# Kernel tuning notes

Hardware: AMD Instinct MI355X
Metric: run time of the kernel (lower is better)

The kernel has to match this reference:

```python
import jax, jax.numpy as jnp
import numpy as np

HARDSHRINK_LAMBDA = 0.75

def setup_inputs() -> dict:
    key = jax.random.key(0)
    k1, k2, k3, k4, k5 = jax.random.split(key, 5)
    B, Cin, H, W = 32, 3, 128, 128
    Cmid, Dout = 256, 4096
    x = jax.random.normal(k1, (B, Cin, H, W), dtype=jnp.float32)
    # Conv2d(3,256,k=3,p=1) params, kaiming-ish scale
    conv_w = jax.random.normal(k2, (Cmid, Cin, 3, 3), dtype=jnp.float32) * (1.0 / np.sqrt(Cin * 9))
    conv_b = jax.random.normal(k3, (Cmid,), dtype=jnp.float32) * 0.01
    fc_w = jax.random.normal(k4, (Dout, Cmid), dtype=jnp.float32) * (1.0 / np.sqrt(Cmid))
    fc_b = jax.random.normal(k5, (Dout,), dtype=jnp.float32) * 0.01
    return {"x": x, "conv_w": conv_w, "conv_b": conv_b, "fc_w": fc_w, "fc_b": fc_b}

def reference(x, conv_w, conv_b, fc_w, fc_b):
    # Conv2d stride=1, padding=1  -> [B, Cmid, H, W]
    y = jax.lax.conv_general_dilated(
        x, conv_w, window_strides=(1, 1), padding=((1, 1), (1, 1)),
        dimension_numbers=("NCHW", "OIHW", "NCHW"))
    y = y + conv_b[None, :, None, None]
    y = jax.nn.relu(y)
    # Nearest upsample (integer scale) replicates each value s*s times; the
    # subsequent elementwise hardshrink then global average pool is therefore
    y = jnp.where(jnp.abs(y) > HARDSHRINK_LAMBDA, y, 0.0)
    pooled = jnp.mean(y, axis=(2, 3))  # [B, Cmid]
    out = pooled @ fc_w.T + fc_b       # [B, Dout]
    return jax.nn.log_sigmoid(out)
```

## Files before the change

kernel.cpp:

```cpp
#include <hip/hip_runtime.h>
#include <hip/hip_bf16.h>

#define LAMBDA 0.75f
#define CMID 256
#define DOUT 4096

typedef __attribute__((ext_vector_type(8))) short bf16x8;
typedef __attribute__((ext_vector_type(4))) float f32x4;

static inline __device__ short f2bf(float f) {
    __hip_bfloat16 h = __float2bfloat16(f);
    short s;
    __builtin_memcpy(&s, &h, 2);
    return s;
}

__global__ void zero_pooled(float* __restrict__ pooled) {
    int i = blockIdx.x * blockDim.x + threadIdx.x;
    if (i < 32 * CMID) pooled[i] = 0.f;
}

__global__ __launch_bounds__(256) void conv_pool_mfma(
    const float* __restrict__ x, const float* __restrict__ conv_w,
    const float* __restrict__ conv_b, float* __restrict__ pooled)
{
    __shared__ float xs[3 * 6 * 132];
    const int b  = blockIdx.x >> 5;
    const int h0 = (blockIdx.x & 31) * 4;
    const int t  = threadIdx.x;
    const int wv = t >> 6;
    const int l  = t & 63;
    const int lm = l & 15;
    const int g  = l >> 4;

    for (int i = t; i < 2376; i += 256) {
        int ci  = i / 792;
        int rem = i - ci * 792;
        int r   = rem / 132;
        int j   = rem - r * 132;
        int hh  = h0 - 1 + r;
        int col = j - 1;
        float v = 0.f;
        if ((unsigned)hh < 128u && (unsigned)col < 128u)
            v = x[(b * 3 + ci) * 16384 + hh * 128 + col];
        xs[i] = v;
    }

    bf16x8 afrag[4];
    f32x4  biasf[4];
    f32x4  pool[4];
    #pragma unroll
    for (int c = 0; c < 4; ++c) {
        const int ct = wv * 4 + c;
        const int co = ct * 16 + lm;
        const float* wp = conv_w + co * 27;
        float av[8];
        if (g < 3) {
            #pragma unroll
            for (int j = 0; j < 8; ++j) av[j] = wp[g * 9 + j];
        } else {
            av[0] = wp[8]; av[1] = wp[17]; av[2] = wp[26];
            av[3] = av[4] = av[5] = av[6] = av[7] = 0.f;
        }
        #pragma unroll
        for (int j = 0; j < 8; ++j) afrag[c][j] = f2bf(av[j]);
        #pragma unroll
        for (int r = 0; r < 4; ++r) {
            biasf[c][r] = conv_b[ct * 16 + 4 * g + r];
            pool[c][r]  = 0.f;
        }
    }

    int off[8];
    if (g < 3) {
        #pragma unroll
        for (int j = 0; j < 8; ++j)
            off[j] = g * 792 + (j / 3) * 132 + (j % 3) - 1;
    } else {
        off[0] = 0 * 792 + 2 * 132 + 1;
        off[1] = 1 * 792 + 2 * 132 + 1;
        off[2] = 2 * 792 + 2 * 132 + 1;
        off[3] = off[4] = off[5] = off[6] = off[7] = 0;
    }

    __syncthreads();

    #pragma unroll
    for (int rr = 0; rr < 4; ++rr) {
        const float* base = xs + rr * 132 + 1 + lm;
        #pragma unroll
        for (int tw = 0; tw < 8; ++tw) {
            float v[8];
            #pragma unroll
            for (int j = 0; j < 8; ++j) v[j] = base[off[j] + tw * 16];
            bf16x8 bfrag;
            #pragma unroll
            for (int j = 0; j < 8; ++j) bfrag[j] = f2bf(v[j]);
            #pragma unroll
            for (int c = 0; c < 4; ++c) {
                f32x4 acc = __builtin_amdgcn_mfma_f32_16x16x32_bf16(
                    afrag[c], bfrag, biasf[c], 0, 0, 0);
                #pragma unroll
                for (int r = 0; r < 4; ++r)
                    pool[c][r] += (acc[r] > LAMBDA) ? acc[r] : 0.f;
            }
        }
    }

    #pragma unroll
    for (int m = 1; m < 16; m <<= 1) {
        #pragma unroll
        for (int c = 0; c < 4; ++c)
            #pragma unroll
            for (int r = 0; r < 4; ++r)
                pool[c][r] += __shfl_xor(pool[c][r], m, 64);
    }
    if (lm == 0) {
        #pragma unroll
        for (int c = 0; c < 4; ++c)
            #pragma unroll
            for (int r = 0; r < 4; ++r)
                atomicAdd(&pooled[b * CMID + (wv * 4 + c) * 16 + 4 * g + r], pool[c][r]);
    }
}

__global__ __launch_bounds__(256) void fc_kernel(
    const float* __restrict__ pooled, const float* __restrict__ fc_w,
    const float* __restrict__ fc_b, float* __restrict__ out)
{
    __shared__ float pool[CMID];
    const int b = blockIdx.y;
    const int t = threadIdx.x;
    pool[t] = pooled[b * CMID + t] * (1.0f / 16384.0f);
    __syncthreads();

    const int d = blockIdx.x * 256 + t;
    const float4* wrow = (const float4*)(fc_w + d * CMID);
    float acc = fc_b[d];
    #pragma unroll 8
    for (int k4 = 0; k4 < CMID / 4; k4++) {
        float4 wv = wrow[k4];
        acc += wv.x * pool[k4 * 4 + 0] + wv.y * pool[k4 * 4 + 1]
             + wv.z * pool[k4 * 4 + 2] + wv.w * pool[k4 * 4 + 3];
    }
    float ls = fminf(acc, 0.f) - log1pf(expf(-fabsf(acc)));
    out[b * (int)DOUT + d] = ls;
}

extern "C" void kernel_launch(void* const* d_in, const int* in_sizes, int n_in,
                              void* d_out, int out_size, void* d_ws, size_t ws_size,
                              hipStream_t stream) {
    const float* x      = (const float*)d_in[0];
    const float* conv_w = (const float*)d_in[1];
    const float* conv_b = (const float*)d_in[2];
    const float* fc_w   = (const float*)d_in[3];
    const float* fc_b   = (const float*)d_in[4];
    float* out = (float*)d_out;

    float* pooled = (float*)d_ws;

    zero_pooled<<<32, 256, 0, stream>>>(pooled);
    conv_pool_mfma<<<32 * 32, 256, 0, stream>>>(x, conv_w, conv_b, pooled);
    fc_kernel<<<dim3(16, 32), 256, 0, stream>>>(pooled, fc_w, fc_b, out);
}
```

Before: 49.50 us.

## Build bf16 im2col tile in LDS and swap MFMA operand roles in conv-pool

The conv kernel now stages a packed bf16 im2col buffer in shared memory, one row per output pixel. Each MFMA B-fragment then comes from a single 16-byte LDS load instead of eight scalar loads and conversions per tile. Operands are swapped so pixels sit on the reduction side, which shrinks the lane reduction to two shuffles, and each block covers two rows instead of four to double the grid. The zero kernel is replaced by hipMemsetAsync, and launch bounds request four blocks per CU, at the cost of an extra LDS pass and sync.

```diff
diff --git a/kernel.cpp b/kernel.cpp
--- a/kernel.cpp
+++ b/kernel.cpp
@@ -10,45 +10,45 @@
 
 static inline __device__ short f2bf(float f) {
     __hip_bfloat16 h = __float2bfloat16(f);
-    short s;
-    __builtin_memcpy(&s, &h, 2);
+    short s; __builtin_memcpy(&s, &h, 2);
     return s;
 }
-
-__global__ void zero_pooled(float* __restrict__ pooled) {
-    int i = blockIdx.x * blockDim.x + threadIdx.x;
-    if (i < 32 * CMID) pooled[i] = 0.f;
+static inline __device__ unsigned pack2(float lo, float hi) {
+    unsigned a = (unsigned short)f2bf(lo);
+    unsigned b = (unsigned short)f2bf(hi);
+    return a | (b << 16);
 }
 
-__global__ __launch_bounds__(256) void conv_pool_mfma(
+__global__ __launch_bounds__(256, 4) void conv_pool_mfma(
     const float* __restrict__ x, const float* __restrict__ conv_w,
     const float* __restrict__ conv_b, float* __restrict__ pooled)
 {
-    __shared__ float xs[3 * 6 * 132];
-    const int b  = blockIdx.x >> 5;
-    const int h0 = (blockIdx.x & 31) * 4;
+    __shared__ float    raw[3 * 4 * 136];
+    __shared__ unsigned im2col[256 * 20];
+
+    const int b  = blockIdx.x >> 6;
+    const int h0 = (blockIdx.x & 63) * 2;
     const int t  = threadIdx.x;
+    const int l  = t & 63;
     const int wv = t >> 6;
-    const int l  = t & 63;
     const int lm = l & 15;
     const int g  = l >> 4;
 
-    for (int i = t; i < 2376; i += 256) {
-        int ci  = i / 792;
-        int rem = i - ci * 792;
-        int r   = rem / 132;
-        int j   = rem - r * 132;
+    for (int i = t; i < 1632; i += 256) {
+        int ci  = i / 544;
+        int rem = i - ci * 544;
+        int r   = rem / 136;
+        int idx = rem - r * 136;
         int hh  = h0 - 1 + r;
-        int col = j - 1;
+        int col = idx - 4;
         float v = 0.f;
         if ((unsigned)hh < 128u && (unsigned)col < 128u)
             v = x[(b * 3 + ci) * 16384 + hh * 128 + col];
-        xs[i] = v;
+        raw[i] = v;
     }
 
-    bf16x8 afrag[4];
-    f32x4  biasf[4];
-    f32x4  pool[4];
+    bf16x8 wfrag[4];
+    f32x4  biasf[4], pool[4];
     #pragma unroll
     for (int c = 0; c < 4; ++c) {
         const int ct = wv * 4 + c;
@@ -63,64 +63,61 @@
             av[3] = av[4] = av[5] = av[6] = av[7] = 0.f;
         }
         #pragma unroll
-        for (int j = 0; j < 8; ++j) afrag[c][j] = f2bf(av[j]);
-        #pragma unroll
-        for (int r = 0; r < 4; ++r) {
-            biasf[c][r] = conv_b[ct * 16 + 4 * g + r];
-            pool[c][r]  = 0.f;
-        }
+        for (int j = 0; j < 8; ++j) wfrag[c][j] = f2bf(av[j]);
+        const float bb = conv_b[co];
+        biasf[c] = (f32x4){bb, bb, bb, bb};
+        pool[c]  = (f32x4){0.f, 0.f, 0.f, 0.f};
     }
 
-    int off[8];
-    if (g < 3) {
+    __syncthreads();
+
+    {
+        const int out_r = t >> 7;
+        const int px    = t & 127;
+        unsigned q[16];
         #pragma unroll
-        for (int j = 0; j < 8; ++j)
-            off[j] = g * 792 + (j / 3) * 132 + (j % 3) - 1;
-    } else {
-        off[0] = 0 * 792 + 2 * 132 + 1;
-        off[1] = 1 * 792 + 2 * 132 + 1;
-        off[2] = 2 * 792 + 2 * 132 + 1;
-        off[3] = off[4] = off[5] = off[6] = off[7] = 0;
+        for (int ci = 0; ci < 3; ++ci) {
+            const float* rp = raw + ci * 544 + out_r * 136 + px + 3;
+            q[ci * 4 + 0] = pack2(rp[0],   rp[1]);
+            q[ci * 4 + 1] = pack2(rp[2],   rp[136]);
+            q[ci * 4 + 2] = pack2(rp[137], rp[138]);
+            q[ci * 4 + 3] = pack2(rp[272], rp[273]);
+        }
+        const float t8c0 = raw[0 * 544 + out_r * 136 + px + 3 + 274];
+        const float t8c1 = raw[1 * 544 + out_r * 136 + px + 3 + 274];
+        const float t8c2 = raw[2 * 544 + out_r * 136 + px + 3 + 274];
+        q[12] = pack2(t8c0, t8c1);
+        q[13] = pack2(t8c2, 0.f);
+        q[14] = 0u; q[15] = 0u;
+        unsigned* dst = &im2col[t * 20];
+        #pragma unroll
+        for (int q4 = 0; q4 < 4; ++q4)
+            *(uint4*)(dst + q4 * 4) = *(const uint4*)(q + q4 * 4);
     }
 
     __syncthreads();
 
     #pragma unroll
-    for (int rr = 0; rr < 4; ++rr) {
-        const float* base = xs + rr * 132 + 1 + lm;
+    for (int tile = 0; tile < 16; ++tile) {
+        const uint4 xr = *(const uint4*)&im2col[(tile * 16 + lm) * 20 + g * 4];
+        bf16x8 xf; __builtin_memcpy(&xf, &xr, 16);
         #pragma unroll
-        for (int tw = 0; tw < 8; ++tw) {
-            float v[8];
+        for (int c = 0; c < 4; ++c) {
+            f32x4 acc = __builtin_amdgcn_mfma_f32_16x16x32_bf16(
+                xf, wfrag[c], biasf[c], 0, 0, 0);
             #pragma unroll
-            for (int j = 0; j < 8; ++j) v[j] = base[off[j] + tw * 16];
-            bf16x8 bfrag;
-            #pragma unroll
-            for (int j = 0; j < 8; ++j) bfrag[j] = f2bf(v[j]);
-            #pragma unroll
-            for (int c = 0; c < 4; ++c) {
-                f32x4 acc = __builtin_amdgcn_mfma_f32_16x16x32_bf16(
-                    afrag[c], bfrag, biasf[c], 0, 0, 0);
-                #pragma unroll
-                for (int r = 0; r < 4; ++r)
-                    pool[c][r] += (acc[r] > LAMBDA) ? acc[r] : 0.f;
-            }
+            for (int r = 0; r < 4; ++r)
+                pool[c][r] += (acc[r] > LAMBDA) ? acc[r] : 0.f;
         }
     }
 
     #pragma unroll
-    for (int m = 1; m < 16; m <<= 1) {
-        #pragma unroll
-        for (int c = 0; c < 4; ++c)
-            #pragma unroll
-            for (int r = 0; r < 4; ++r)
-                pool[c][r] += __shfl_xor(pool[c][r], m, 64);
-    }
-    if (lm == 0) {
-        #pragma unroll
-        for (int c = 0; c < 4; ++c)
-            #pragma unroll
-            for (int r = 0; r < 4; ++r)
-                atomicAdd(&pooled[b * CMID + (wv * 4 + c) * 16 + 4 * g + r], pool[c][r]);
+    for (int c = 0; c < 4; ++c) {
+        float s = (pool[c][0] + pool[c][1]) + (pool[c][2] + pool[c][3]);
+        s += __shfl_xor(s, 16, 64);
+        s += __shfl_xor(s, 32, 64);
+        if (l < 16)
+            atomicAdd(&pooled[b * CMID + (wv * 4 + c) * 16 + lm], s);
     }
 }
 
@@ -159,7 +156,7 @@
 
     float* pooled = (float*)d_ws;
 
-    zero_pooled<<<32, 256, 0, stream>>>(pooled);
-    conv_pool_mfma<<<32 * 32, 256, 0, stream>>>(x, conv_w, conv_b, pooled);
+    hipMemsetAsync(pooled, 0, 32 * CMID * sizeof(float), stream);
+    conv_pool_mfma<<<32 * 64, 256, 0, stream>>>(x, conv_w, conv_b, pooled);
     fc_kernel<<<dim3(16, 32), 256, 0, stream>>>(pooled, fc_w, fc_b, out);
 }
```

Result: slower. 97.40 us (+96.8%).
